# Kernel optimization log

Hardware: AMD Instinct MI355X
Metric: run time of the kernel (lower is better)

## Reference

```python
import jax, jax.numpy as jnp
import numpy as np

N_NODES = 100000
N_EDGES = 3200000
N_FEAT = 128
N_GRAPHS = 64


def setup_inputs() -> dict:
    key = jax.random.key(0)
    ks = jax.random.split(key, 8)
    x = jax.random.normal(ks[0], (N_NODES, N_FEAT), dtype=jnp.float32)
    edge_index = jax.random.randint(ks[1], (2, N_EDGES), 0, N_NODES, dtype=jnp.int64)
    batch = jnp.sort(jax.random.randint(ks[2], (N_NODES,), 0, N_GRAPHS, dtype=jnp.int64))
    # GCNConv weights (glorot-style scale) and biases
    W1 = jax.random.normal(ks[3], (N_FEAT, 32), dtype=jnp.float32) / np.sqrt(N_FEAT)
    b1 = jnp.zeros((32,), dtype=jnp.float32)
    W2 = jax.random.normal(ks[4], (32, 16), dtype=jnp.float32) / np.sqrt(32.0)
    b2 = jnp.zeros((16,), dtype=jnp.float32)
    lin_w = jax.random.normal(ks[5], (16, 1), dtype=jnp.float32) / np.sqrt(16.0)
    lin_b = jnp.zeros((1,), dtype=jnp.float32)
    return {"x": x, "edge_index": edge_index, "batch": batch,
            "W1": W1, "b1": b1, "W2": W2, "b2": b2,
            "lin_w": lin_w, "lin_b": lin_b}


def _gcn_conv(x, W, b, src, dst, deg_inv_sqrt, n_nodes):
    # transform first (fewer features downstream when out_dim < in_dim)
    xw = x @ W  # [N, out]
    norm = deg_inv_sqrt[src] * deg_inv_sqrt[dst]  # [E+N]
    msg = xw[src] * norm[:, None]  # gather + scale
    out = jax.ops.segment_sum(msg, dst, num_segments=n_nodes)  # scatter-add
    return out + b


def reference(x, edge_index, batch, W1, b1, W2, b2, lin_w, lin_b):
    n_nodes = x.shape[0]
    self_loop = jnp.arange(n_nodes, dtype=edge_index.dtype)
    src = jnp.concatenate([edge_index[0], self_loop])
    dst = jnp.concatenate([edge_index[1], self_loop])
    # symmetric GCN normalization with self-loops
    deg = jax.ops.segment_sum(jnp.ones_like(src, dtype=x.dtype), dst,
                              num_segments=n_nodes)
    deg_inv_sqrt = jnp.where(deg > 0, jax.lax.rsqrt(jnp.maximum(deg, 1.0)), 0.0)

    h = _gcn_conv(x, W1, b1, src, dst, deg_inv_sqrt, n_nodes)
    h = jax.nn.relu(h)
    # F.dropout with training=False (eval) is identity
    h = _gcn_conv(h, W2, b2, src, dst, deg_inv_sqrt, n_nodes)

    # global_mean_pool over batch index
    sums = jax.ops.segment_sum(h, batch, num_segments=N_GRAPHS)  # [G,16]
    cnts = jax.ops.segment_sum(jnp.ones((n_nodes,), dtype=h.dtype), batch,
                               num_segments=N_GRAPHS)
    pooled = sums / jnp.maximum(cnts, 1.0)[:, None]
    return pooled @ lin_w + lin_b  # [G,1]
```

## Files before the change

kernel.cpp:

```cpp
#include <hip/hip_runtime.h>

#define NN 100000
#define NE 3200000
#define NF 128
#define C1 32
#define C2 16
#define NG 64
#define BKT_SH 7
#define BKT_W  128
#define NBKT   782
#define CH     8192
#define NW     391
#define RSTR   784
#define MAPCAP 6400

#define OFF_BCNT  0
#define OFF_BST   1024
#define OFF_RUN   2048
#define OFF_ROW   308608
#define OFF_DIS   408624
#define OFF_POOL  508624
#define OFF_CNTF  509648
#define OFF_EDG   509712
#define OFF_XS1   OFF_EDG
#define OFF_XS2B  (OFF_EDG + NE)
#define OFF_COL   (OFF_XS2B + NN*8)

__device__ __forceinline__ unsigned pack_bf2(float a, float b) {
    unsigned ua = __float_as_uint(a);
    unsigned ub = __float_as_uint(b);
    ua = (ua + 0x7fffu + ((ua >> 16) & 1u)) >> 16;
    ub = (ub + 0x7fffu + ((ub >> 16) & 1u)) & 0xffff0000u;
    return ua | ub;
}
__device__ __forceinline__ float2 unpack_bf2(unsigned u) {
    return make_float2(__uint_as_float(u << 16), __uint_as_float(u & 0xffff0000u));
}
__device__ __forceinline__ void acc4(float4& a, uint2 q) {
    float2 f0 = unpack_bf2(q.x), f1 = unpack_bf2(q.y);
    a.x += f0.x; a.y += f0.y; a.z += f1.x; a.w += f1.y;
}

__global__ __launch_bounds__(512) void k_part(
    const int* __restrict__ S, const int* __restrict__ D,
    unsigned* __restrict__ edgebuf, int* __restrict__ runstart,
    int* __restrict__ bcnt)
{
    __shared__ int lhist[1024];
    __shared__ int lstart[1024];
    __shared__ int lcur[NBKT];
    __shared__ int wsum[8];
    __shared__ unsigned lsort[CH];
    const int w = blockIdx.x;
    const int t = threadIdx.x;
    const int e0 = w * CH;
    const int n = min(CH, NE - e0);

    for (int i = t; i < 1024; i += 512) lhist[i] = 0;
    __syncthreads();
    for (int i = t; i < n; i += 512)
        atomicAdd(&lhist[(unsigned)D[e0 + i] >> BKT_SH], 1);
    __syncthreads();
    for (int i = t; i < NBKT; i += 512) atomicAdd(&bcnt[i], lhist[i]);

    int c0 = lhist[t * 2 + 0], c1 = lhist[t * 2 + 1];
    int ts = c0 + c1;
    const int lane = t & 63, wv = t >> 6;
    int sc = ts;
    #pragma unroll
    for (int off = 1; off < 64; off <<= 1) {
        int v = __shfl_up(sc, off, 64);
        if (lane >= off) sc += v;
    }
    if (lane == 63) wsum[wv] = sc;
    __syncthreads();
    int wo = 0;
    #pragma unroll
    for (int i = 0; i < 8; ++i) wo += (i < wv) ? wsum[i] : 0;
    int excl = sc - ts + wo;
    lstart[t * 2 + 0] = excl;
    lstart[t * 2 + 1] = excl + c0;
    __syncthreads();

    for (int i = t; i < 783; i += 512) runstart[w * RSTR + i] = lstart[i];
    for (int i = t; i < NBKT; i += 512) lcur[i] = lstart[i];
    __syncthreads();
    for (int i = t; i < n; i += 512) {
        int s = S[e0 + i], d = D[e0 + i];
        int pos = atomicAdd(&lcur[(unsigned)d >> BKT_SH], 1);
        lsort[pos] = ((unsigned)s << BKT_SH) | (unsigned)(d & (BKT_W - 1));
    }
    __syncthreads();
    for (int i = t; i < n; i += 512) edgebuf[e0 + i] = lsort[i];
}

__global__ __launch_bounds__(256) void k_bscan(const int* __restrict__ bcnt,
                                               int* __restrict__ bstart,
                                               int* __restrict__ rowstart) {
    __shared__ int sd[256];
    const int t = threadIdx.x;
    const int base = t * 4;
    int c0 = (base + 0 < NBKT) ? bcnt[base + 0] : 0;
    int c1 = (base + 1 < NBKT) ? bcnt[base + 1] : 0;
    int c2 = (base + 2 < NBKT) ? bcnt[base + 2] : 0;
    int c3 = (base + 3 < NBKT) ? bcnt[base + 3] : 0;
    int ts = c0 + c1 + c2 + c3;
    sd[t] = ts;
    __syncthreads();
    for (int off = 1; off < 256; off <<= 1) {
        int v = (t >= off) ? sd[t - off] : 0;
        __syncthreads();
        sd[t] += v;
        __syncthreads();
    }
    int excl = sd[t] - ts;
    if (base + 0 < 783) bstart[base + 0] = excl;
    if (base + 1 < 783) bstart[base + 1] = excl + c0;
    if (base + 2 < 783) bstart[base + 2] = excl + c0 + c1;
    if (base + 3 < 783) bstart[base + 3] = excl + c0 + c1 + c2;
    if (t == 0) rowstart[NN] = NE;
}

__global__ __launch_bounds__(256) void k_fillfused(
    const unsigned* __restrict__ edgebuf, const int* __restrict__ runstart,
    const int* __restrict__ bstart,
    int* __restrict__ rowstart, float* __restrict__ dis, int* __restrict__ colidx)
{
    __shared__ int rl[NW];
    __shared__ int pfx[NW];
    __shared__ int basea[NW];
    __shared__ unsigned short map[MAPCAP];
    __shared__ int lcnt[BKT_W];
    __shared__ int lcur[BKT_W];
    __shared__ int sd[256];
    const int b = blockIdx.x;
    const int t = threadIdx.x;
    const int bs = bstart[b];
    const int total = bstart[b + 1] - bs;

    for (int w = t; w < NW; w += 256) {
        int s0 = runstart[w * RSTR + b];
        int s1 = runstart[w * RSTR + b + 1];
        basea[w] = s0;
        rl[w] = s1 - s0;
    }
    if (t < BKT_W) lcnt[t] = 0;
    __syncthreads();
    {
        int w0 = t * 2;
        int c0 = (w0 < NW) ? rl[w0] : 0;
        int c1 = (w0 + 1 < NW) ? rl[w0 + 1] : 0;
        int ts = c0 + c1;
        sd[t] = ts;
        __syncthreads();
        for (int off = 1; off < 256; off <<= 1) {
            int v = (t >= off) ? sd[t - off] : 0;
            __syncthreads();
            sd[t] += v;
            __syncthreads();
        }
        int excl = sd[t] - ts;
        if (w0 < NW)     pfx[w0]     = excl;
        if (w0 + 1 < NW) pfx[w0 + 1] = excl + c0;
    }
    __syncthreads();
    for (int w = t; w < NW; w += 256) {
        int p = pfx[w], len = rl[w];
        basea[w] = w * CH + basea[w] - p;
        for (int i = 0; i < len; ++i) map[p + i] = (unsigned short)w;
    }
    __syncthreads();
    for (int j = t; j < total; j += 256) {
        unsigned p = edgebuf[basea[map[j]] + j];
        atomicAdd(&lcnt[p & (BKT_W - 1)], 1);
    }
    __syncthreads();
    if (t < BKT_W) lcur[t] = lcnt[t];
    __syncthreads();
    for (int off = 1; off < BKT_W; off <<= 1) {
        int v = (t < BKT_W && t >= off) ? lcur[t - off] : 0;
        __syncthreads();
        if (t < BKT_W) lcur[t] += v;
        __syncthreads();
    }
    if (t < BKT_W) {
        int excl = lcur[t] - lcnt[t];
        int node = b * BKT_W + t;
        if (node < NN) {
            rowstart[node] = bs + excl;
            dis[node] = rsqrtf((float)lcnt[t] + 1.0f);
        }
        lcur[t] = bs + excl;
    }
    __syncthreads();
    for (int j = t; j < total; j += 256) {
        unsigned p = edgebuf[basea[map[j]] + j];
        int pos = atomicAdd(&lcur[p & (BKT_W - 1)], 1);
        colidx[pos] = (int)(p >> BKT_SH);
    }
}

__global__ __launch_bounds__(256) void k_gemm1(
    const float* __restrict__ x, const float* __restrict__ W1,
    const float* __restrict__ dis,
    unsigned* __restrict__ xs1)
{
    __shared__ float xls[128 * 33];
    __shared__ float wls[32 * 32];
    const int t = threadIdx.x;
    const int tc = t & 7;
    const int tr = t >> 3;
    const int base = blockIdx.x * 128;

    float a[4][4] = {};

    for (int k0 = 0; k0 < NF; k0 += 32) {
        {
            int i = t * 4;
            int kk = i >> 5, c = i & 31;
            *(float4*)&wls[kk * 32 + c] = *(const float4*)&W1[(k0 + kk) * C1 + c];
        }
        #pragma unroll
        for (int r = 0; r < 4; ++r) {
            int n = (t >> 3) + r * 32;
            int j = (t & 7) * 4;
            int node = base + n;
            float4 v = make_float4(0.f, 0.f, 0.f, 0.f);
            if (node < NN) v = *(const float4*)&x[(long long)node * NF + k0 + j];
            xls[n * 33 + j + 0] = v.x;
            xls[n * 33 + j + 1] = v.y;
            xls[n * 33 + j + 2] = v.z;
            xls[n * 33 + j + 3] = v.w;
        }
        __syncthreads();
        #pragma unroll 8
        for (int kk = 0; kk < 32; ++kk) {
            float4 w = *(const float4*)&wls[kk * 32 + tc * 4];
            #pragma unroll
            for (int i = 0; i < 4; ++i) {
                float xv = xls[(tr * 4 + i) * 33 + kk];
                a[i][0] = fmaf(xv, w.x, a[i][0]);
                a[i][1] = fmaf(xv, w.y, a[i][1]);
                a[i][2] = fmaf(xv, w.z, a[i][2]);
                a[i][3] = fmaf(xv, w.w, a[i][3]);
            }
        }
        __syncthreads();
    }
    #pragma unroll
    for (int i = 0; i < 4; ++i) {
        int node = base + tr * 4 + i;
        if (node < NN) {
            float dv = dis[node];
            uint2 o;
            o.x = pack_bf2(a[i][0] * dv, a[i][1] * dv);
            o.y = pack_bf2(a[i][2] * dv, a[i][3] * dv);
            *(uint2*)&xs1[node * 16 + tc * 2] = o;
        }
    }
}

__global__ __launch_bounds__(256) void k_gather1(
    const unsigned* __restrict__ xs1, const int* __restrict__ colidx,
    const int* __restrict__ rowstart, const float* __restrict__ dis,
    const float* __restrict__ b1, const float* __restrict__ W2,
    unsigned* __restrict__ xs2b)
{
    __shared__ float w2s[C1 * C2];
    __shared__ float hrow[32 * 33];
    const int t = threadIdx.x;
    if (t < 128) *(float4*)&w2s[t * 4] = *(const float4*)&W2[t * 4];
    const int l = t & 7;
    const int n = t >> 3;
    const int v = blockIdx.x * 32 + n;

    const int start = rowstart[v];
    const int num = rowstart[v + 1] - start;
    const int* __restrict__ cp = &colidx[start];
    uint2 u = *(const uint2*)&xs1[v * 16 + l * 2];
    float4 a0 = make_float4(0.f, 0.f, 0.f, 0.f);
    acc4(a0, u);
    float4 a1 = make_float4(0.f, 0.f, 0.f, 0.f), a2 = a1, a3 = a1;
    int i = 0;
    for (; i + 8 <= num; i += 8) {
        int s0 = cp[i], s1 = cp[i+1], s2 = cp[i+2], s3 = cp[i+3];
        int s4 = cp[i+4], s5 = cp[i+5], s6 = cp[i+6], s7 = cp[i+7];
        uint2 q0 = *(const uint2*)&xs1[s0 * 16 + l * 2];
        uint2 q1 = *(const uint2*)&xs1[s1 * 16 + l * 2];
        uint2 q2 = *(const uint2*)&xs1[s2 * 16 + l * 2];
        uint2 q3 = *(const uint2*)&xs1[s3 * 16 + l * 2];
        uint2 q4 = *(const uint2*)&xs1[s4 * 16 + l * 2];
        uint2 q5 = *(const uint2*)&xs1[s5 * 16 + l * 2];
        uint2 q6 = *(const uint2*)&xs1[s6 * 16 + l * 2];
        uint2 q7 = *(const uint2*)&xs1[s7 * 16 + l * 2];
        acc4(a0, q0); acc4(a1, q1); acc4(a2, q2); acc4(a3, q3);
        acc4(a0, q4); acc4(a1, q5); acc4(a2, q6); acc4(a3, q7);
    }
    for (; i < num; ++i) {
        uint2 q = *(const uint2*)&xs1[cp[i] * 16 + l * 2];
        acc4(a0, q);
    }
    float ax = (a0.x + a1.x) + (a2.x + a3.x);
    float ay = (a0.y + a1.y) + (a2.y + a3.y);
    float az = (a0.z + a1.z) + (a2.z + a3.z);
    float aw = (a0.w + a1.w) + (a2.w + a3.w);
    const float dv = dis[v];

    hrow[n * 33 + l * 4 + 0] = fmaxf(fmaf(ax, dv, b1[l * 4 + 0]), 0.f);
    hrow[n * 33 + l * 4 + 1] = fmaxf(fmaf(ay, dv, b1[l * 4 + 1]), 0.f);
    hrow[n * 33 + l * 4 + 2] = fmaxf(fmaf(az, dv, b1[l * 4 + 2]), 0.f);
    hrow[n * 33 + l * 4 + 3] = fmaxf(fmaf(aw, dv, b1[l * 4 + 3]), 0.f);
    __syncthreads();

    const float* hr = &hrow[n * 33];
    float s0 = 0.f, s1 = 0.f;
    #pragma unroll
    for (int k = 0; k < 32; ++k) {
        float hv = hr[k];
        s0 = fmaf(hv, w2s[k * C2 + 2 * l + 0], s0);
        s1 = fmaf(hv, w2s[k * C2 + 2 * l + 1], s1);
    }
    xs2b[v * 8 + l] = pack_bf2(s0 * dv, s1 * dv);
}

__global__ __launch_bounds__(256) void k_gather2(
    const unsigned* __restrict__ xs2b, const int* __restrict__ colidx,
    const int* __restrict__ rowstart, const float* __restrict__ dis,
    const int* __restrict__ batch,
    float* __restrict__ pool, float* __restrict__ cntf)
{
    __shared__ float psum[NG * C2];
    __shared__ float cs[NG];
    const int t = threadIdx.x;
    for (int i = t; i < NG * C2; i += 256) psum[i] = 0.f;
    if (t < NG) cs[t] = 0.f;
    __syncthreads();

    const int l = t & 3;
    const int n = t >> 2;
    const int v = blockIdx.x * 64 + n;
    if (v < NN) {
        const int start = rowstart[v];
        const int num = rowstart[v + 1] - start;
        const int* __restrict__ cp = &colidx[start];
        uint2 u = *(const uint2*)&xs2b[v * 8 + l * 2];
        float4 a0 = make_float4(0.f, 0.f, 0.f, 0.f);
        acc4(a0, u);
        float4 a1 = make_float4(0.f, 0.f, 0.f, 0.f), a2 = a1, a3 = a1;
        int i = 0;
        for (; i + 8 <= num; i += 8) {
            int s0 = cp[i], s1 = cp[i+1], s2 = cp[i+2], s3 = cp[i+3];
            int s4 = cp[i+4], s5 = cp[i+5], s6 = cp[i+6], s7 = cp[i+7];
            uint2 q0 = *(const uint2*)&xs2b[s0 * 8 + l * 2];
            uint2 q1 = *(const uint2*)&xs2b[s1 * 8 + l * 2];
            uint2 q2 = *(const uint2*)&xs2b[s2 * 8 + l * 2];
            uint2 q3 = *(const uint2*)&xs2b[s3 * 8 + l * 2];
            uint2 q4 = *(const uint2*)&xs2b[s4 * 8 + l * 2];
            uint2 q5 = *(const uint2*)&xs2b[s5 * 8 + l * 2];
            uint2 q6 = *(const uint2*)&xs2b[s6 * 8 + l * 2];
            uint2 q7 = *(const uint2*)&xs2b[s7 * 8 + l * 2];
            acc4(a0, q0); acc4(a1, q1); acc4(a2, q2); acc4(a3, q3);
            acc4(a0, q4); acc4(a1, q5); acc4(a2, q6); acc4(a3, q7);
        }
        for (; i < num; ++i) {
            uint2 q = *(const uint2*)&xs2b[cp[i] * 8 + l * 2];
            acc4(a0, q);
        }
        float ax = (a0.x + a1.x) + (a2.x + a3.x);
        float ay = (a0.y + a1.y) + (a2.y + a3.y);
        float az = (a0.z + a1.z) + (a2.z + a3.z);
        float aw = (a0.w + a1.w) + (a2.w + a3.w);
        float dv = dis[v];
        int g = batch[v];
        atomicAdd(&psum[g * C2 + l * 4 + 0], ax * dv);
        atomicAdd(&psum[g * C2 + l * 4 + 1], ay * dv);
        atomicAdd(&psum[g * C2 + l * 4 + 2], az * dv);
        atomicAdd(&psum[g * C2 + l * 4 + 3], aw * dv);
        if (l == 0) atomicAdd(&cs[g], 1.0f);
    }
    __syncthreads();
    for (int i = t; i < NG * C2; i += 256)
        if (psum[i] != 0.f) atomicAdd(&pool[i], psum[i]);
    if (t < NG && cs[t] != 0.f) atomicAdd(&cntf[t], cs[t]);
}

__global__ void k_final(const float* __restrict__ pool, const float* __restrict__ cntf,
                        const float* __restrict__ b2,
                        const float* __restrict__ lw, const float* __restrict__ lb,
                        float* __restrict__ out)
{
    int g = threadIdx.x;
    if (g < NG) {
        float c = fmaxf(cntf[g], 1.0f);
        float inv = 1.0f / c;
        float s = lb[0];
        #pragma unroll
        for (int k = 0; k < C2; ++k) {
            s = fmaf(b2[k], lw[k], s);
            s = fmaf(pool[g * C2 + k] * inv, lw[k], s);
        }
        out[g] = s;
    }
}

extern "C" void kernel_launch(void* const* d_in, const int* in_sizes, int n_in,
                              void* d_out, int out_size, void* d_ws, size_t ws_size,
                              hipStream_t stream) {
    const float* x     = (const float*)d_in[0];
    const int*   ei    = (const int*)d_in[1];
    const int*   batch = (const int*)d_in[2];
    const float* W1    = (const float*)d_in[3];
    const float* b1    = (const float*)d_in[4];
    const float* W2    = (const float*)d_in[5];
    const float* b2    = (const float*)d_in[6];
    const float* lw    = (const float*)d_in[7];
    const float* lb    = (const float*)d_in[8];
    float* out = (float*)d_out;

    float*    wsf = (float*)d_ws;
    int*      wsi = (int*)d_ws;
    unsigned* wsu = (unsigned*)d_ws;

    int*      bcnt     = wsi + OFF_BCNT;
    int*      bstart   = wsi + OFF_BST;
    int*      runstart = wsi + OFF_RUN;
    int*      rowstart = wsi + OFF_ROW;
    float*    dis      = wsf + OFF_DIS;
    float*    pool     = wsf + OFF_POOL;
    float*    cntf     = wsf + OFF_CNTF;
    unsigned* edgebuf  = wsu + OFF_EDG;
    unsigned* xs1      = wsu + OFF_XS1;
    unsigned* xs2b     = wsu + OFF_XS2B;
    int*      colidx   = wsi + OFF_COL;

    const int* S = ei;
    const int* D = ei + NE;

    hipMemsetAsync(bcnt, 0, 1024 * sizeof(int), stream);
    hipMemsetAsync(pool, 0, (NG * C2 + NG) * sizeof(float), stream);

    k_part       <<<NW, 512, 0, stream>>>(S, D, edgebuf, runstart, bcnt);
    k_bscan      <<<1, 256, 0, stream>>>(bcnt, bstart, rowstart);
    k_fillfused  <<<NBKT, 256, 0, stream>>>(edgebuf, runstart, bstart, rowstart, dis, colidx);
    k_gemm1      <<<(NN + 127) / 128, 256, 0, stream>>>(x, W1, dis, xs1);
    k_gather1    <<<NN / 32, 256, 0, stream>>>(xs1, colidx, rowstart, dis, b1, W2, xs2b);
    k_gather2    <<<(NN + 63) / 64, 256, 0, stream>>>(xs2b, colidx, rowstart, dis, batch, pool, cntf);
    k_final      <<<1, 64, 0, stream>>>(pool, cntf, b2, lw, lb, out);
}
```

Before: 257.2 us.

## Vectorize edge loads, fold bucket scan into fill, widen gathers, warp-reduce pooling

```diff
diff --git a/kernel.cpp b/kernel.cpp
--- a/kernel.cpp
+++ b/kernel.cpp
@@ -15,13 +15,12 @@
 #define MAPCAP 6400
 
 #define OFF_BCNT  0
-#define OFF_BST   1024
-#define OFF_RUN   2048
-#define OFF_ROW   308608
-#define OFF_DIS   408624
-#define OFF_POOL  508624
-#define OFF_CNTF  509648
-#define OFF_EDG   509712
+#define OFF_POOL  1024
+#define OFF_CNTF  2048
+#define OFF_RUN   2304
+#define OFF_ROW   308848
+#define OFF_DIS   408864
+#define OFF_EDG   508864
 #define OFF_XS1   OFF_EDG
 #define OFF_XS2B  (OFF_EDG + NE)
 #define OFF_COL   (OFF_XS2B + NN*8)
@@ -36,9 +35,11 @@
 __device__ __forceinline__ float2 unpack_bf2(unsigned u) {
     return make_float2(__uint_as_float(u << 16), __uint_as_float(u & 0xffff0000u));
 }
-__device__ __forceinline__ void acc4(float4& a, uint2 q) {
+__device__ __forceinline__ void accum8(float* a, uint4 q) {
     float2 f0 = unpack_bf2(q.x), f1 = unpack_bf2(q.y);
-    a.x += f0.x; a.y += f0.y; a.z += f1.x; a.w += f1.y;
+    float2 f2 = unpack_bf2(q.z), f3 = unpack_bf2(q.w);
+    a[0] += f0.x; a[1] += f0.y; a[2] += f1.x; a[3] += f1.y;
+    a[4] += f2.x; a[5] += f2.y; a[6] += f3.x; a[7] += f3.y;
 }
 
 __global__ __launch_bounds__(512) void k_part(
@@ -55,11 +56,19 @@
     const int t = threadIdx.x;
     const int e0 = w * CH;
     const int n = min(CH, NE - e0);
+    const int n4 = n >> 2;
+    const int4* __restrict__ S4 = (const int4*)(S + e0);
+    const int4* __restrict__ D4 = (const int4*)(D + e0);
 
     for (int i = t; i < 1024; i += 512) lhist[i] = 0;
     __syncthreads();
-    for (int i = t; i < n; i += 512)
-        atomicAdd(&lhist[(unsigned)D[e0 + i] >> BKT_SH], 1);
+    for (int i = t; i < n4; i += 512) {
+        int4 d = D4[i];
+        atomicAdd(&lhist[(unsigned)d.x >> BKT_SH], 1);
+        atomicAdd(&lhist[(unsigned)d.y >> BKT_SH], 1);
+        atomicAdd(&lhist[(unsigned)d.z >> BKT_SH], 1);
+        atomicAdd(&lhist[(unsigned)d.w >> BKT_SH], 1);
+    }
     __syncthreads();
     for (int i = t; i < NBKT; i += 512) atomicAdd(&bcnt[i], lhist[i]);
 
@@ -85,45 +94,29 @@
     for (int i = t; i < 783; i += 512) runstart[w * RSTR + i] = lstart[i];
     for (int i = t; i < NBKT; i += 512) lcur[i] = lstart[i];
     __syncthreads();
-    for (int i = t; i < n; i += 512) {
-        int s = S[e0 + i], d = D[e0 + i];
-        int pos = atomicAdd(&lcur[(unsigned)d >> BKT_SH], 1);
-        lsort[pos] = ((unsigned)s << BKT_SH) | (unsigned)(d & (BKT_W - 1));
-    }
-    __syncthreads();
-    for (int i = t; i < n; i += 512) edgebuf[e0 + i] = lsort[i];
-}
-
-__global__ __launch_bounds__(256) void k_bscan(const int* __restrict__ bcnt,
-                                               int* __restrict__ bstart,
-                                               int* __restrict__ rowstart) {
-    __shared__ int sd[256];
-    const int t = threadIdx.x;
-    const int base = t * 4;
-    int c0 = (base + 0 < NBKT) ? bcnt[base + 0] : 0;
-    int c1 = (base + 1 < NBKT) ? bcnt[base + 1] : 0;
-    int c2 = (base + 2 < NBKT) ? bcnt[base + 2] : 0;
-    int c3 = (base + 3 < NBKT) ? bcnt[base + 3] : 0;
-    int ts = c0 + c1 + c2 + c3;
-    sd[t] = ts;
-    __syncthreads();
-    for (int off = 1; off < 256; off <<= 1) {
-        int v = (t >= off) ? sd[t - off] : 0;
-        __syncthreads();
-        sd[t] += v;
-        __syncthreads();
-    }
-    int excl = sd[t] - ts;
-    if (base + 0 < 783) bstart[base + 0] = excl;
-    if (base + 1 < 783) bstart[base + 1] = excl + c0;
-    if (base + 2 < 783) bstart[base + 2] = excl + c0 + c1;
-    if (base + 3 < 783) bstart[base + 3] = excl + c0 + c1 + c2;
-    if (t == 0) rowstart[NN] = NE;
+    for (int i = t; i < n4; i += 512) {
+        int4 s = S4[i];
+        int4 d = D4[i];
+        { int p = atomicAdd(&lcur[(unsigned)d.x >> BKT_SH], 1);
+          lsort[p] = ((unsigned)s.x << BKT_SH) | ((unsigned)d.x & (BKT_W - 1)); }
+        { int p = atomicAdd(&lcur[(unsigned)d.y >> BKT_SH], 1);
+          lsort[p] = ((unsigned)s.y << BKT_SH) | ((unsigned)d.y & (BKT_W - 1)); }
+        { int p = atomicAdd(&lcur[(unsigned)d.z >> BKT_SH], 1);
+          lsort[p] = ((unsigned)s.z << BKT_SH) | ((unsigned)d.z & (BKT_W - 1)); }
+        { int p = atomicAdd(&lcur[(unsigned)d.w >> BKT_SH], 1);
+          lsort[p] = ((unsigned)s.w << BKT_SH) | ((unsigned)d.w & (BKT_W - 1)); }
+    }
+    __syncthreads();
+    {
+        uint4* __restrict__ eb4 = (uint4*)(edgebuf + e0);
+        const uint4* __restrict__ ls4 = (const uint4*)lsort;
+        for (int i = t; i < n4; i += 512) eb4[i] = ls4[i];
+    }
 }
 
 __global__ __launch_bounds__(256) void k_fillfused(
     const unsigned* __restrict__ edgebuf, const int* __restrict__ runstart,
-    const int* __restrict__ bstart,
+    const int* __restrict__ bcnt,
     int* __restrict__ rowstart, float* __restrict__ dis, int* __restrict__ colidx)
 {
     __shared__ int rl[NW];
@@ -132,11 +125,17 @@
     __shared__ unsigned short map[MAPCAP];
     __shared__ int lcnt[BKT_W];
     __shared__ int lcur[BKT_W];
-    __shared__ int sd[256];
+    __shared__ int wsum[4];
+    __shared__ int hs1;
     const int b = blockIdx.x;
     const int t = threadIdx.x;
-    const int bs = bstart[b];
-    const int total = bstart[b + 1] - bs;
+    const int lane = t & 63, wv = t >> 6;
+
+    int accp = 0;
+    for (int i = t; i < b; i += 256) accp += bcnt[i];
+    #pragma unroll
+    for (int off = 1; off < 64; off <<= 1) accp += __shfl_xor(accp, off, 64);
+    if (lane == 0) wsum[wv] = accp;
 
     for (int w = t; w < NW; w += 256) {
         int s0 = runstart[w * RSTR + b];
@@ -146,24 +145,30 @@
     }
     if (t < BKT_W) lcnt[t] = 0;
     __syncthreads();
-    {
-        int w0 = t * 2;
-        int c0 = (w0 < NW) ? rl[w0] : 0;
-        int c1 = (w0 + 1 < NW) ? rl[w0 + 1] : 0;
-        int ts = c0 + c1;
-        sd[t] = ts;
-        __syncthreads();
-        for (int off = 1; off < 256; off <<= 1) {
-            int v = (t >= off) ? sd[t - off] : 0;
-            __syncthreads();
-            sd[t] += v;
-            __syncthreads();
-        }
-        int excl = sd[t] - ts;
-        if (w0 < NW)     pfx[w0]     = excl;
-        if (w0 + 1 < NW) pfx[w0 + 1] = excl + c0;
-    }
-    __syncthreads();
+    const int bs = wsum[0] + wsum[1] + wsum[2] + wsum[3];
+
+    int w0 = t * 2;
+    int c0 = (w0 < NW) ? rl[w0] : 0;
+    int c1 = (w0 + 1 < NW) ? rl[w0 + 1] : 0;
+    int ts = c0 + c1;
+    int sc = ts;
+    #pragma unroll
+    for (int off = 1; off < 64; off <<= 1) {
+        int v = __shfl_up(sc, off, 64);
+        if (lane >= off) sc += v;
+    }
+    __syncthreads();
+    if (lane == 63) wsum[wv] = sc;
+    __syncthreads();
+    int wo = 0;
+    #pragma unroll
+    for (int i = 0; i < 4; ++i) wo += (i < wv) ? wsum[i] : 0;
+    const int total = wsum[0] + wsum[1] + wsum[2] + wsum[3];
+    int excl0 = sc - ts + wo;
+    if (w0 < NW)     pfx[w0]     = excl0;
+    if (w0 + 1 < NW) pfx[w0 + 1] = excl0 + c0;
+    __syncthreads();
+
     for (int w = t; w < NW; w += 256) {
         int p = pfx[w], len = rl[w];
         basea[w] = w * CH + basea[w] - p;
@@ -175,23 +180,29 @@
         atomicAdd(&lcnt[p & (BKT_W - 1)], 1);
     }
     __syncthreads();
-    if (t < BKT_W) lcur[t] = lcnt[t];
-    __syncthreads();
-    for (int off = 1; off < BKT_W; off <<= 1) {
-        int v = (t < BKT_W && t >= off) ? lcur[t - off] : 0;
-        __syncthreads();
-        if (t < BKT_W) lcur[t] += v;
-        __syncthreads();
-    }
+
+    int myc = 0, sc2 = 0;
     if (t < BKT_W) {
-        int excl = lcur[t] - lcnt[t];
+        myc = lcnt[t];
+        sc2 = myc;
+        #pragma unroll
+        for (int off = 1; off < 64; off <<= 1) {
+            int v = __shfl_up(sc2, off, 64);
+            if (lane >= off) sc2 += v;
+        }
+        if (t == 63) hs1 = sc2;
+    }
+    __syncthreads();
+    if (t < BKT_W) {
+        int excl = sc2 - myc + ((t >= 64) ? hs1 : 0);
         int node = b * BKT_W + t;
         if (node < NN) {
             rowstart[node] = bs + excl;
-            dis[node] = rsqrtf((float)lcnt[t] + 1.0f);
+            dis[node] = rsqrtf((float)myc + 1.0f);
         }
         lcur[t] = bs + excl;
     }
+    if (b == 0 && t == 0) rowstart[NN] = NE;
     __syncthreads();
     for (int j = t; j < total; j += 256) {
         unsigned p = edgebuf[basea[map[j]] + j];
@@ -267,60 +278,62 @@
     unsigned* __restrict__ xs2b)
 {
     __shared__ float w2s[C1 * C2];
-    __shared__ float hrow[32 * 33];
+    __shared__ float hrow[64 * 33];
     const int t = threadIdx.x;
     if (t < 128) *(float4*)&w2s[t * 4] = *(const float4*)&W2[t * 4];
-    const int l = t & 7;
-    const int n = t >> 3;
-    const int v = blockIdx.x * 32 + n;
-
-    const int start = rowstart[v];
-    const int num = rowstart[v + 1] - start;
-    const int* __restrict__ cp = &colidx[start];
-    uint2 u = *(const uint2*)&xs1[v * 16 + l * 2];
-    float4 a0 = make_float4(0.f, 0.f, 0.f, 0.f);
-    acc4(a0, u);
-    float4 a1 = make_float4(0.f, 0.f, 0.f, 0.f), a2 = a1, a3 = a1;
-    int i = 0;
-    for (; i + 8 <= num; i += 8) {
-        int s0 = cp[i], s1 = cp[i+1], s2 = cp[i+2], s3 = cp[i+3];
-        int s4 = cp[i+4], s5 = cp[i+5], s6 = cp[i+6], s7 = cp[i+7];
-        uint2 q0 = *(const uint2*)&xs1[s0 * 16 + l * 2];
-        uint2 q1 = *(const uint2*)&xs1[s1 * 16 + l * 2];
-        uint2 q2 = *(const uint2*)&xs1[s2 * 16 + l * 2];
-        uint2 q3 = *(const uint2*)&xs1[s3 * 16 + l * 2];
-        uint2 q4 = *(const uint2*)&xs1[s4 * 16 + l * 2];
-        uint2 q5 = *(const uint2*)&xs1[s5 * 16 + l * 2];
-        uint2 q6 = *(const uint2*)&xs1[s6 * 16 + l * 2];
-        uint2 q7 = *(const uint2*)&xs1[s7 * 16 + l * 2];
-        acc4(a0, q0); acc4(a1, q1); acc4(a2, q2); acc4(a3, q3);
-        acc4(a0, q4); acc4(a1, q5); acc4(a2, q6); acc4(a3, q7);
-    }
-    for (; i < num; ++i) {
-        uint2 q = *(const uint2*)&xs1[cp[i] * 16 + l * 2];
-        acc4(a0, q);
-    }
-    float ax = (a0.x + a1.x) + (a2.x + a3.x);
-    float ay = (a0.y + a1.y) + (a2.y + a3.y);
-    float az = (a0.z + a1.z) + (a2.z + a3.z);
-    float aw = (a0.w + a1.w) + (a2.w + a3.w);
-    const float dv = dis[v];
-
-    hrow[n * 33 + l * 4 + 0] = fmaxf(fmaf(ax, dv, b1[l * 4 + 0]), 0.f);
-    hrow[n * 33 + l * 4 + 1] = fmaxf(fmaf(ay, dv, b1[l * 4 + 1]), 0.f);
-    hrow[n * 33 + l * 4 + 2] = fmaxf(fmaf(az, dv, b1[l * 4 + 2]), 0.f);
-    hrow[n * 33 + l * 4 + 3] = fmaxf(fmaf(aw, dv, b1[l * 4 + 3]), 0.f);
-    __syncthreads();
-
-    const float* hr = &hrow[n * 33];
-    float s0 = 0.f, s1 = 0.f;
-    #pragma unroll
-    for (int k = 0; k < 32; ++k) {
-        float hv = hr[k];
-        s0 = fmaf(hv, w2s[k * C2 + 2 * l + 0], s0);
-        s1 = fmaf(hv, w2s[k * C2 + 2 * l + 1], s1);
-    }
-    xs2b[v * 8 + l] = pack_bf2(s0 * dv, s1 * dv);
+    const int l = t & 3;
+    const int n = t >> 2;
+    const int v = blockIdx.x * 64 + n;
+    const bool valid = v < NN;
+
+    float a0[8] = {}, a1[8] = {};
+    float dv = 0.f;
+    if (valid) {
+        const int start = rowstart[v];
+        const int num = rowstart[v + 1] - start;
+        const int* __restrict__ cp = &colidx[start];
+        const uint4* __restrict__ tb = (const uint4*)xs1;
+        accum8(a0, tb[v * 4 + l]);
+        int i = 0;
+        for (; i + 8 <= num; i += 8) {
+            int s0 = cp[i],   s1 = cp[i+1], s2 = cp[i+2], s3 = cp[i+3];
+            int s4 = cp[i+4], s5 = cp[i+5], s6 = cp[i+6], s7 = cp[i+7];
+            uint4 q0 = tb[s0 * 4 + l];
+            uint4 q1 = tb[s1 * 4 + l];
+            uint4 q2 = tb[s2 * 4 + l];
+            uint4 q3 = tb[s3 * 4 + l];
+            uint4 q4 = tb[s4 * 4 + l];
+            uint4 q5 = tb[s5 * 4 + l];
+            uint4 q6 = tb[s6 * 4 + l];
+            uint4 q7 = tb[s7 * 4 + l];
+            accum8(a0, q0); accum8(a1, q1); accum8(a0, q2); accum8(a1, q3);
+            accum8(a0, q4); accum8(a1, q5); accum8(a0, q6); accum8(a1, q7);
+        }
+        for (; i < num; ++i) accum8(a0, tb[cp[i] * 4 + l]);
+        dv = dis[v];
+        #pragma unroll
+        for (int j = 0; j < 8; ++j) {
+            float h = fmaxf(fmaf(a0[j] + a1[j], dv, b1[l * 8 + j]), 0.f);
+            hrow[n * 33 + l * 8 + j] = h;
+        }
+    }
+    __syncthreads();
+    if (valid) {
+        const float* hr = &hrow[n * 33];
+        float s0 = 0.f, s1 = 0.f, s2 = 0.f, s3 = 0.f;
+        #pragma unroll
+        for (int k = 0; k < 32; ++k) {
+            float hv = hr[k];
+            s0 = fmaf(hv, w2s[k * C2 + l * 4 + 0], s0);
+            s1 = fmaf(hv, w2s[k * C2 + l * 4 + 1], s1);
+            s2 = fmaf(hv, w2s[k * C2 + l * 4 + 2], s2);
+            s3 = fmaf(hv, w2s[k * C2 + l * 4 + 3], s3);
+        }
+        uint2 o;
+        o.x = pack_bf2(s0 * dv, s1 * dv);
+        o.y = pack_bf2(s2 * dv, s3 * dv);
+        *(uint2*)&xs2b[v * 8 + l * 2] = o;
+    }
 }
 
 __global__ __launch_bounds__(256) void k_gather2(
@@ -336,47 +349,65 @@
     if (t < NG) cs[t] = 0.f;
     __syncthreads();
 
-    const int l = t & 3;
-    const int n = t >> 2;
-    const int v = blockIdx.x * 64 + n;
-    if (v < NN) {
+    const int l = t & 1;
+    const int n = t >> 1;
+    const int v = blockIdx.x * 128 + n;
+    const bool valid = v < NN;
+    const int lane = t & 63;
+
+    float r[8] = {};
+    int g = 0;
+    if (valid) {
         const int start = rowstart[v];
         const int num = rowstart[v + 1] - start;
         const int* __restrict__ cp = &colidx[start];
-        uint2 u = *(const uint2*)&xs2b[v * 8 + l * 2];
-        float4 a0 = make_float4(0.f, 0.f, 0.f, 0.f);
-        acc4(a0, u);
-        float4 a1 = make_float4(0.f, 0.f, 0.f, 0.f), a2 = a1, a3 = a1;
+        const uint4* __restrict__ tb = (const uint4*)xs2b;
+        float a0[8] = {}, a1[8] = {};
+        accum8(a0, tb[v * 2 + l]);
         int i = 0;
         for (; i + 8 <= num; i += 8) {
-            int s0 = cp[i], s1 = cp[i+1], s2 = cp[i+2], s3 = cp[i+3];
+            int s0 = cp[i],   s1 = cp[i+1], s2 = cp[i+2], s3 = cp[i+3];
             int s4 = cp[i+4], s5 = cp[i+5], s6 = cp[i+6], s7 = cp[i+7];
-            uint2 q0 = *(const uint2*)&xs2b[s0 * 8 + l * 2];
-            uint2 q1 = *(const uint2*)&xs2b[s1 * 8 + l * 2];
-            uint2 q2 = *(const uint2*)&xs2b[s2 * 8 + l * 2];
-            uint2 q3 = *(const uint2*)&xs2b[s3 * 8 + l * 2];
-            uint2 q4 = *(const uint2*)&xs2b[s4 * 8 + l * 2];
-            uint2 q5 = *(const uint2*)&xs2b[s5 * 8 + l * 2];
-            uint2 q6 = *(const uint2*)&xs2b[s6 * 8 + l * 2];
-            uint2 q7 = *(const uint2*)&xs2b[s7 * 8 + l * 2];
-            acc4(a0, q0); acc4(a1, q1); acc4(a2, q2); acc4(a3, q3);
-            acc4(a0, q4); acc4(a1, q5); acc4(a2, q6); acc4(a3, q7);
-        }
-        for (; i < num; ++i) {
-            uint2 q = *(const uint2*)&xs2b[cp[i] * 8 + l * 2];
-            acc4(a0, q);
-        }
-        float ax = (a0.x + a1.x) + (a2.x + a3.x);
-        float ay = (a0.y + a1.y) + (a2.y + a3.y);
-        float az = (a0.z + a1.z) + (a2.z + a3.z);
-        float aw = (a0.w + a1.w) + (a2.w + a3.w);
+            uint4 q0 = tb[s0 * 2 + l];
+            uint4 q1 = tb[s1 * 2 + l];
+            uint4 q2 = tb[s2 * 2 + l];
+            uint4 q3 = tb[s3 * 2 + l];
+            uint4 q4 = tb[s4 * 2 + l];
+            uint4 q5 = tb[s5 * 2 + l];
+            uint4 q6 = tb[s6 * 2 + l];
+            uint4 q7 = tb[s7 * 2 + l];
+            accum8(a0, q0); accum8(a1, q1); accum8(a0, q2); accum8(a1, q3);
+            accum8(a0, q4); accum8(a1, q5); accum8(a0, q6); accum8(a1, q7);
+        }
+        for (; i < num; ++i) accum8(a0, tb[cp[i] * 2 + l]);
         float dv = dis[v];
-        int g = batch[v];
-        atomicAdd(&psum[g * C2 + l * 4 + 0], ax * dv);
-        atomicAdd(&psum[g * C2 + l * 4 + 1], ay * dv);
-        atomicAdd(&psum[g * C2 + l * 4 + 2], az * dv);
-        atomicAdd(&psum[g * C2 + l * 4 + 3], aw * dv);
-        if (l == 0) atomicAdd(&cs[g], 1.0f);
+        g = batch[v];
+        #pragma unroll
+        for (int j = 0; j < 8; ++j) r[j] = (a0[j] + a1[j]) * dv;
+    }
+
+    int g0 = __shfl(g, 0, 64);
+    bool uni = __all(!valid || g == g0);
+    if (uni) {
+        #pragma unroll
+        for (int j = 0; j < 8; ++j) {
+            float val = r[j];
+            val += __shfl_xor(val, 2, 64);
+            val += __shfl_xor(val, 4, 64);
+            val += __shfl_xor(val, 8, 64);
+            val += __shfl_xor(val, 16, 64);
+            val += __shfl_xor(val, 32, 64);
+            if (lane < 2) atomicAdd(&psum[g0 * C2 + lane * 8 + j], val);
+        }
+        unsigned long long mb = __ballot(valid && (l == 0));
+        if (lane == 0 && mb) atomicAdd(&cs[g0], (float)__popcll(mb));
+    } else {
+        if (valid) {
+            #pragma unroll
+            for (int j = 0; j < 8; ++j)
+                atomicAdd(&psum[g * C2 + l * 8 + j], r[j]);
+            if (l == 0) atomicAdd(&cs[g], 1.0f);
+        }
     }
     __syncthreads();
     for (int i = t; i < NG * C2; i += 256)
@@ -422,12 +453,11 @@
     unsigned* wsu = (unsigned*)d_ws;
 
     int*      bcnt     = wsi + OFF_BCNT;
-    int*      bstart   = wsi + OFF_BST;
+    float*    pool     = wsf + OFF_POOL;
+    float*    cntf     = wsf + OFF_CNTF;
     int*      runstart = wsi + OFF_RUN;
     int*      rowstart = wsi + OFF_ROW;
     float*    dis      = wsf + OFF_DIS;
-    float*    pool     = wsf + OFF_POOL;
-    float*    cntf     = wsf + OFF_CNTF;
     unsigned* edgebuf  = wsu + OFF_EDG;
     unsigned* xs1      = wsu + OFF_XS1;
     unsigned* xs2b     = wsu + OFF_XS2B;
@@ -436,14 +466,12 @@
     const int* S = ei;
     const int* D = ei + NE;
 
-    hipMemsetAsync(bcnt, 0, 1024 * sizeof(int), stream);
-    hipMemsetAsync(pool, 0, (NG * C2 + NG) * sizeof(float), stream);
+    hipMemsetAsync(wsi + OFF_BCNT, 0, 2304 * sizeof(int), stream);
 
     k_part       <<<NW, 512, 0, stream>>>(S, D, edgebuf, runstart, bcnt);
-    k_bscan      <<<1, 256, 0, stream>>>(bcnt, bstart, rowstart);
-    k_fillfused  <<<NBKT, 256, 0, stream>>>(edgebuf, runstart, bstart, rowstart, dis, colidx);
+    k_fillfused  <<<NBKT, 256, 0, stream>>>(edgebuf, runstart, bcnt, rowstart, dis, colidx);
     k_gemm1      <<<(NN + 127) / 128, 256, 0, stream>>>(x, W1, dis, xs1);
-    k_gather1    <<<NN / 32, 256, 0, stream>>>(xs1, colidx, rowstart, dis, b1, W2, xs2b);
-    k_gather2    <<<(NN + 63) / 64, 256, 0, stream>>>(xs2b, colidx, rowstart, dis, batch, pool, cntf);
+    k_gather1    <<<(NN + 63) / 64, 256, 0, stream>>>(xs1, colidx, rowstart, dis, b1, W2, xs2b);
+    k_gather2    <<<(NN + 127) / 128, 256, 0, stream>>>(xs2b, colidx, rowstart, dis, batch, pool, cntf);
     k_final      <<<1, 64, 0, stream>>>(pool, cntf, b2, lw, lb, out);
 }
```

Result: faster. 251.2 us (-2.3%).
